# Optimization experiments

Hardware: AMD Instinct MI355X
Metric: run time of the kernel (lower is better)

The kernel has to match this reference:

```python
import jax, jax.numpy as jnp
import numpy as np

SCALE = 1.0

def setup_inputs() -> dict:
    key = jax.random.key(0)
    k1, k2 = jax.random.split(key)
    features = jax.random.normal(k1, (16, 512, 128, 128), dtype=jnp.float32)
    probs = jax.random.normal(k2, (16, 19, 128, 128), dtype=jnp.float32)
    return {"features": features, "probs": probs}

def reference(features, probs):
    B, K, H, W = probs.shape
    C = features.shape[1]
    p = probs.reshape(B, K, H * W)               # [B, K, HW]
    f = features.reshape(B, C, H * W)            # [B, C, HW]
    attn = jax.nn.softmax(SCALE * p, axis=2)     # softmax over spatial dim
    # ocr_context[b, k, c] = sum_hw attn[b,k,hw] * f[b,c,hw]
    ctx = jnp.einsum('bks,bcs->bkc', attn, f)    # [B, K, C]
    return jnp.transpose(ctx, (0, 2, 1))[..., None]  # [B, C, K, 1]
```

## Files before the change

### kernel.cpp

```cpp
#include <hip/hip_runtime.h>
#include <math.h>

#define BATCH 16
#define KCLS  19
#define CCH   512
#define HW    16384

#define KSPLIT 16
#define KB     (HW / KSPLIT)
#define BK     64
#define NCHUNK (KB / BK)
#define NT     128
#define KPAD   20
#define BCN    (BATCH * CCH)

typedef __attribute__((ext_vector_type(8))) short  short8;
typedef __attribute__((ext_vector_type(4))) short  short4v;
typedef __attribute__((ext_vector_type(4))) float  floatx4;

static __device__ __forceinline__ ushort f2bf(float x) {
  unsigned u = __float_as_uint(x);
  return (ushort)((u + 0x7FFFu + ((u >> 16) & 1u)) >> 16);
}

static __device__ __forceinline__ short8 pack8(floatx4 a, floatx4 b) {
  short8 v;
  v[0] = (short)f2bf(a[0]); v[1] = (short)f2bf(a[1]);
  v[2] = (short)f2bf(a[2]); v[3] = (short)f2bf(a[3]);
  v[4] = (short)f2bf(b[0]); v[5] = (short)f2bf(b[1]);
  v[6] = (short)f2bf(b[2]); v[7] = (short)f2bf(b[3]);
  return v;
}

__global__ __launch_bounds__(256) void softmax_stats_kernel(
    const float* __restrict__ probs, float* __restrict__ stats) {
  const int bk = blockIdx.x;
  const float4* row = (const float4*)(probs + (size_t)bk * HW);
  const int tid  = threadIdx.x;
  const int lane = tid & 63;
  const int wave = tid >> 6;
  __shared__ float red[4];

  float s = 0.f;
  for (int i = tid; i < HW / 4; i += 256) {
    float4 v = row[i];
    s += __expf(v.x) + __expf(v.y) + __expf(v.z) + __expf(v.w);
  }
  for (int off = 32; off > 0; off >>= 1) s += __shfl_xor(s, off);
  if (lane == 0) red[wave] = s;
  __syncthreads();
  if (tid == 0) {
    float total = red[0] + red[1] + red[2] + red[3];
    stats[2 * bk]     = 0.0f;
    stats[2 * bk + 1] = 1.0f / total;
  }
}

struct FSet { floatx4 v[8]; };

__global__ __launch_bounds__(256, 2) void gather_mfma(
    const float* __restrict__ feat, const float* __restrict__ probs,
    const float* __restrict__ stats, float* __restrict__ part) {
  __shared__ __align__(16) short A_all[KCLS][KB];

  const int bid = blockIdx.x;
  const int b   = bid & 15;
  const int r1  = bid >> 4;
  const int ct  = r1 & 3;
  const int ks  = r1 >> 2;
  const int k0  = ks * KB;

  const int tid  = threadIdx.x;
  const int wave = tid >> 6;
  const int lane = tid & 63;

  const float* fbase = feat  + ((size_t)(b * CCH + ct * NT)) * HW + k0;
  const float* pbase = probs + ((size_t)b * KCLS) * HW + k0;

  const int ch0 = wave * 32 + (lane & 15);
  const int ch1 = ch0 + 16;
  const float* fptr0 = fbase + (size_t)ch0 * HW + (lane >> 4) * 8;
  const float* fptr1 = fbase + (size_t)ch1 * HW + (lane >> 4) * 8;

  floatx4 acc00 = {0,0,0,0}, acc01 = {0,0,0,0}, acc10 = {0,0,0,0}, acc11 = {0,0,0,0};

  FSet sA, sB;

#define LOADF(S, c)                                                             \
  {                                                                             \
    const int cb = (c) * BK;                                                    \
    S.v[0] = *(const floatx4*)(fptr0 + cb);                                     \
    S.v[1] = *(const floatx4*)(fptr0 + cb + 4);                                 \
    S.v[2] = *(const floatx4*)(fptr1 + cb);                                     \
    S.v[3] = *(const floatx4*)(fptr1 + cb + 4);                                 \
    S.v[4] = *(const floatx4*)(fptr0 + cb + 32);                                \
    S.v[5] = *(const floatx4*)(fptr0 + cb + 36);                                \
    S.v[6] = *(const floatx4*)(fptr1 + cb + 32);                                \
    S.v[7] = *(const floatx4*)(fptr1 + cb + 36);                                \
  }

#define GEMMC(S, c)                                                             \
  {                                                                             \
    const char* Ab = (const char*)A_all;                                        \
    const int rm0  = lane & 15;                                                 \
    const int rm1  = 16 + (rm0 < 3 ? rm0 : 2);    \
    _Pragma("unroll")                                                           \
    for (int kt = 0; kt < 2; kt++) {                                            \
      const int g = (c) * 8 + kt * 4 + (lane >> 4);                             \
      short8 a0 = *(const short8*)(Ab + rm0 * 2048 + ((g ^ (rm0 & 7)) << 4));   \
      short8 a1 = *(const short8*)(Ab + rm1 * 2048 + ((g ^ (rm1 & 7)) << 4));   \
      short8 b0 = pack8(S.v[kt * 4 + 0], S.v[kt * 4 + 1]);                      \
      short8 b1 = pack8(S.v[kt * 4 + 2], S.v[kt * 4 + 3]);                      \
      acc00 = __builtin_amdgcn_mfma_f32_16x16x32_bf16(a0, b0, acc00, 0, 0, 0);  \
      acc01 = __builtin_amdgcn_mfma_f32_16x16x32_bf16(a0, b1, acc01, 0, 0, 0);  \
      acc10 = __builtin_amdgcn_mfma_f32_16x16x32_bf16(a1, b0, acc10, 0, 0, 0);  \
      acc11 = __builtin_amdgcn_mfma_f32_16x16x32_bf16(a1, b1, acc11, 0, 0, 0);  \
    }                                                                           \
  }

  LOADF(sA, 0);

  for (int j = 0; j < KCLS; j++) {
    float m  = stats[2 * (b * KCLS + j)];
    float iv = stats[2 * (b * KCLS + j) + 1];
    float4 p = *(const float4*)(pbase + (size_t)j * HW + tid * 4);
    short4v v;
    v[0] = (short)f2bf(__expf(p.x - m) * iv);
    v[1] = (short)f2bf(__expf(p.y - m) * iv);
    v[2] = (short)f2bf(__expf(p.z - m) * iv);
    v[3] = (short)f2bf(__expf(p.w - m) * iv);
    *(short4v*)((char*)A_all + j * 2048 + (((tid >> 1) ^ (j & 7)) << 4) + (tid & 1) * 8) = v;
  }
  __syncthreads();

  for (int c = 0; c < NCHUNK; c += 2) {
    LOADF(sB, c + 1);
    GEMMC(sA, c);
    if (c + 2 < NCHUNK) LOADF(sA, c + 2);
    GEMMC(sB, c + 1);
  }

  {
    const int chb = ct * NT + wave * 32;
    const int cl  = lane & 15;
    const int rb  = (lane >> 4) * 4;
    size_t bc0 = (size_t)b * CCH + chb + cl;
    size_t bc1 = bc0 + 16;
    float* p0 = part + ((size_t)ks * BCN + bc0) * KPAD + rb;
    float* p1 = part + ((size_t)ks * BCN + bc1) * KPAD + rb;
    *(floatx4*)p0 = acc00;
    *(floatx4*)p1 = acc01;
    if (rb == 0) {
      *(floatx4*)(p0 + 16) = acc10;
      *(floatx4*)(p1 + 16) = acc11;
    }
  }
#undef LOADF
#undef GEMMC
}

__global__ __launch_bounds__(256) void reduce_kernel(
    const float* __restrict__ part, float* __restrict__ out) {
  const int gid = blockIdx.x * 256 + threadIdx.x;
  const int bc = gid / KPAD, r = gid - bc * KPAD;
  if (r < KCLS) {
    float s = 0.f;
    #pragma unroll
    for (int k = 0; k < KSPLIT; k++)
      s += part[(size_t)k * (BCN * KPAD) + gid];
    out[(size_t)bc * KCLS + r] = s;
  }
}

extern "C" void kernel_launch(void* const* d_in, const int* in_sizes, int n_in,
                              void* d_out, int out_size, void* d_ws, size_t ws_size,
                              hipStream_t stream) {
  const float* feat  = (const float*)d_in[0];
  const float* probs = (const float*)d_in[1];
  float* out   = (float*)d_out;
  float* stats = (float*)d_ws;
  float* part  = (float*)((char*)d_ws + 4096);

  softmax_stats_kernel<<<BATCH * KCLS, 256, 0, stream>>>(probs, stats);
  gather_mfma<<<BATCH * 4 * KSPLIT, 256, 0, stream>>>(feat, probs, stats, part);
  reduce_kernel<<<(BCN * KPAD) / 256, 256, 0, stream>>>(part, out);
}
```

Before: 134.9 us.

## Fuse softmax normalization into gather kernel and defer division to reduce

```diff
diff --git a/kernel.cpp b/kernel.cpp
--- a/kernel.cpp
+++ b/kernel.cpp
@@ -15,53 +15,30 @@
 #define BCN    (BATCH * CCH)
 
 typedef __attribute__((ext_vector_type(8))) short  short8;
-typedef __attribute__((ext_vector_type(4))) short  short4v;
 typedef __attribute__((ext_vector_type(4))) float  floatx4;
 
-static __device__ __forceinline__ ushort f2bf(float x) {
-  unsigned u = __float_as_uint(x);
-  return (ushort)((u + 0x7FFFu + ((u >> 16) & 1u)) >> 16);
+static __device__ __forceinline__ unsigned cvt_pk(float lo, float hi) {
+  unsigned r;
+  asm("v_cvt_pk_bf16_f32 %0, %1, %2" : "=v"(r) : "v"(lo), "v"(hi));
+  return r;
 }
 
 static __device__ __forceinline__ short8 pack8(floatx4 a, floatx4 b) {
-  short8 v;
-  v[0] = (short)f2bf(a[0]); v[1] = (short)f2bf(a[1]);
-  v[2] = (short)f2bf(a[2]); v[3] = (short)f2bf(a[3]);
-  v[4] = (short)f2bf(b[0]); v[5] = (short)f2bf(b[1]);
-  v[6] = (short)f2bf(b[2]); v[7] = (short)f2bf(b[3]);
-  return v;
-}
-
-__global__ __launch_bounds__(256) void softmax_stats_kernel(
-    const float* __restrict__ probs, float* __restrict__ stats) {
-  const int bk = blockIdx.x;
-  const float4* row = (const float4*)(probs + (size_t)bk * HW);
-  const int tid  = threadIdx.x;
-  const int lane = tid & 63;
-  const int wave = tid >> 6;
-  __shared__ float red[4];
-
-  float s = 0.f;
-  for (int i = tid; i < HW / 4; i += 256) {
-    float4 v = row[i];
-    s += __expf(v.x) + __expf(v.y) + __expf(v.z) + __expf(v.w);
-  }
-  for (int off = 32; off > 0; off >>= 1) s += __shfl_xor(s, off);
-  if (lane == 0) red[wave] = s;
-  __syncthreads();
-  if (tid == 0) {
-    float total = red[0] + red[1] + red[2] + red[3];
-    stats[2 * bk]     = 0.0f;
-    stats[2 * bk + 1] = 1.0f / total;
-  }
+  union { unsigned u[4]; short8 s; } x;
+  x.u[0] = cvt_pk(a[0], a[1]);
+  x.u[1] = cvt_pk(a[2], a[3]);
+  x.u[2] = cvt_pk(b[0], b[1]);
+  x.u[3] = cvt_pk(b[2], b[3]);
+  return x.s;
 }
 
 struct FSet { floatx4 v[8]; };
 
 __global__ __launch_bounds__(256, 2) void gather_mfma(
     const float* __restrict__ feat, const float* __restrict__ probs,
-    const float* __restrict__ stats, float* __restrict__ part) {
+    float* __restrict__ pws, float* __restrict__ part) {
   __shared__ __align__(16) short A_all[KCLS][KB];
+  __shared__ float red[KCLS][4];
 
   const int bid = blockIdx.x;
   const int b   = bid & 15;
@@ -121,17 +98,26 @@
   LOADF(sA, 0);
 
   for (int j = 0; j < KCLS; j++) {
-    float m  = stats[2 * (b * KCLS + j)];
-    float iv = stats[2 * (b * KCLS + j) + 1];
     float4 p = *(const float4*)(pbase + (size_t)j * HW + tid * 4);
-    short4v v;
-    v[0] = (short)f2bf(__expf(p.x - m) * iv);
-    v[1] = (short)f2bf(__expf(p.y - m) * iv);
-    v[2] = (short)f2bf(__expf(p.z - m) * iv);
-    v[3] = (short)f2bf(__expf(p.w - m) * iv);
-    *(short4v*)((char*)A_all + j * 2048 + (((tid >> 1) ^ (j & 7)) << 4) + (tid & 1) * 8) = v;
+    float e0 = __expf(p.x), e1 = __expf(p.y), e2 = __expf(p.z), e3 = __expf(p.w);
+    union { unsigned u[2]; } x;
+    x.u[0] = cvt_pk(e0, e1);
+    x.u[1] = cvt_pk(e2, e3);
+    *(unsigned long long*)((char*)A_all + j * 2048 +
+                           (((tid >> 1) ^ (j & 7)) << 4) + (tid & 1) * 8) =
+        ((unsigned long long)x.u[1] << 32) | x.u[0];
+    if (ct == 0) {
+      float s = e0 + e1 + e2 + e3;
+      for (int off = 32; off > 0; off >>= 1) s += __shfl_xor(s, off);
+      if (lane == 0) red[j][wave] = s;
+    }
   }
   __syncthreads();
+
+  if (ct == 0 && tid < KCLS) {
+    float tot = red[tid][0] + red[tid][1] + red[tid][2] + red[tid][3];
+    pws[(b * KCLS + tid) * KSPLIT + ks] = tot;
+  }
 
   for (int c = 0; c < NCHUNK; c += 2) {
     LOADF(sB, c + 1);
@@ -160,15 +146,21 @@
 }
 
 __global__ __launch_bounds__(256) void reduce_kernel(
-    const float* __restrict__ part, float* __restrict__ out) {
+    const float* __restrict__ part, const float* __restrict__ pws,
+    float* __restrict__ out) {
   const int gid = blockIdx.x * 256 + threadIdx.x;
   const int bc = gid / KPAD, r = gid - bc * KPAD;
   if (r < KCLS) {
+    const int b = bc >> 9;
+    float se = 0.f;
+    #pragma unroll
+    for (int k = 0; k < KSPLIT; k++)
+      se += pws[(b * KCLS + r) * KSPLIT + k];
     float s = 0.f;
     #pragma unroll
     for (int k = 0; k < KSPLIT; k++)
       s += part[(size_t)k * (BCN * KPAD) + gid];
-    out[(size_t)bc * KCLS + r] = s;
+    out[(size_t)bc * KCLS + r] = s / se;
   }
 }
 
@@ -177,11 +169,10 @@
                               hipStream_t stream) {
   const float* feat  = (const float*)d_in[0];
   const float* probs = (const float*)d_in[1];
-  float* out   = (float*)d_out;
-  float* stats = (float*)d_ws;
-  float* part  = (float*)((char*)d_ws + 4096);
+  float* out  = (float*)d_out;
+  float* pws  = (float*)d_ws;
+  float* part = (float*)((char*)d_ws + 32768);
 
-  softmax_stats_kernel<<<BATCH * KCLS, 256, 0, stream>>>(probs, stats);
-  gather_mfma<<<BATCH * 4 * KSPLIT, 256, 0, stream>>>(feat, probs, stats, part);
-  reduce_kernel<<<(BCN * KPAD) / 256, 256, 0, stream>>>(part, out);
+  gather_mfma<<<BATCH * 4 * KSPLIT, 256, 0, stream>>>(feat, probs, pws, part);
+  reduce_kernel<<<(BCN * KPAD) / 256, 256, 0, stream>>>(part, pws, out);
 }
```

After: 142.9 us. 5.9% more time.

## Use one 1024-thread block per batch/k-split covering all channels

Applied to the files above, without the earlier changes.

```diff
diff --git a/kernel.cpp b/kernel.cpp
--- a/kernel.cpp
+++ b/kernel.cpp
@@ -10,12 +10,11 @@
 #define KB     (HW / KSPLIT)
 #define BK     64
 #define NCHUNK (KB / BK)
-#define NT     128
+#define NT     512
 #define KPAD   20
 #define BCN    (BATCH * CCH)
 
 typedef __attribute__((ext_vector_type(8))) short  short8;
-typedef __attribute__((ext_vector_type(4))) short  short4v;
 typedef __attribute__((ext_vector_type(4))) float  floatx4;
 
 static __device__ __forceinline__ ushort f2bf(float x) {
@@ -58,23 +57,21 @@
 
 struct FSet { floatx4 v[8]; };
 
-__global__ __launch_bounds__(256, 2) void gather_mfma(
+__global__ __launch_bounds__(1024, 2) void gather_mfma(
     const float* __restrict__ feat, const float* __restrict__ probs,
     const float* __restrict__ stats, float* __restrict__ part) {
   __shared__ __align__(16) short A_all[KCLS][KB];
 
   const int bid = blockIdx.x;
   const int b   = bid & 15;
-  const int r1  = bid >> 4;
-  const int ct  = r1 & 3;
-  const int ks  = r1 >> 2;
+  const int ks  = bid >> 4;
   const int k0  = ks * KB;
 
   const int tid  = threadIdx.x;
   const int wave = tid >> 6;
   const int lane = tid & 63;
 
-  const float* fbase = feat  + ((size_t)(b * CCH + ct * NT)) * HW + k0;
+  const float* fbase = feat  + ((size_t)b * CCH) * HW + k0;
   const float* pbase = probs + ((size_t)b * KCLS) * HW + k0;
 
   const int ch0 = wave * 32 + (lane & 15);
@@ -120,16 +117,23 @@
 
   LOADF(sA, 0);
 
-  for (int j = 0; j < KCLS; j++) {
+  for (int idx = tid; idx < KCLS * 256; idx += 1024) {
+    const int j = idx >> 8;
+    const int t = idx & 255;
     float m  = stats[2 * (b * KCLS + j)];
     float iv = stats[2 * (b * KCLS + j) + 1];
-    float4 p = *(const float4*)(pbase + (size_t)j * HW + tid * 4);
-    short4v v;
-    v[0] = (short)f2bf(__expf(p.x - m) * iv);
-    v[1] = (short)f2bf(__expf(p.y - m) * iv);
-    v[2] = (short)f2bf(__expf(p.z - m) * iv);
-    v[3] = (short)f2bf(__expf(p.w - m) * iv);
-    *(short4v*)((char*)A_all + j * 2048 + (((tid >> 1) ^ (j & 7)) << 4) + (tid & 1) * 8) = v;
+    float4 p = *(const float4*)(pbase + (size_t)j * HW + t * 4);
+    unsigned long long w;
+    {
+      ushort e0 = f2bf(__expf(p.x - m) * iv);
+      ushort e1 = f2bf(__expf(p.y - m) * iv);
+      ushort e2 = f2bf(__expf(p.z - m) * iv);
+      ushort e3 = f2bf(__expf(p.w - m) * iv);
+      w = (unsigned long long)e0 | ((unsigned long long)e1 << 16) |
+          ((unsigned long long)e2 << 32) | ((unsigned long long)e3 << 48);
+    }
+    *(unsigned long long*)((char*)A_all + j * 2048 +
+                           (((t >> 1) ^ (j & 7)) << 4) + (t & 1) * 8) = w;
   }
   __syncthreads();
 
@@ -141,7 +145,7 @@
   }
 
   {
-    const int chb = ct * NT + wave * 32;
+    const int chb = wave * 32;
     const int cl  = lane & 15;
     const int rb  = (lane >> 4) * 4;
     size_t bc0 = (size_t)b * CCH + chb + cl;
@@ -182,6 +186,6 @@
   float* part  = (float*)((char*)d_ws + 4096);
 
   softmax_stats_kernel<<<BATCH * KCLS, 256, 0, stream>>>(probs, stats);
-  gather_mfma<<<BATCH * 4 * KSPLIT, 256, 0, stream>>>(feat, probs, stats, part);
+  gather_mfma<<<BATCH * KSPLIT, 1024, 0, stream>>>(feat, probs, stats, part);
   reduce_kernel<<<(BCN * KPAD) / 256, 256, 0, stream>>>(part, out);
 }
```

Result: faster. 130.2 us (-3.5%).
